# Kernel optimization log

Hardware: AMD Instinct MI355X
Metric: run time of the kernel (lower is better)

Reference implementation:

```python
import jax, jax.numpy as jnp
import numpy as np

F_FRAMES = 128   # number of frames (seq_start_end rows)
P_PEDS = 32      # pedestrians per frame (uniform)
B = F_FRAMES * P_PEDS
E, H, BN, PM, M = 64, 128, 1024, 512, 1024
PRED_LEN = 12


def setup_inputs() -> dict:
    key = jax.random.key(0)
    ks = jax.random.split(key, 20)
    n = lambda k, s, sc=0.05: (jax.random.normal(k, s) * sc).astype(jnp.float32)
    starts = jnp.arange(F_FRAMES, dtype=jnp.int32) * P_PEDS
    seq_start_end = jnp.stack([starts, starts + P_PEDS], axis=1)
    return {
        "h0": n(ks[0], (1, B, H), 1.0),
        "c0": n(ks[1], (1, B, H), 1.0),
        "obs_final_pos": n(ks[2], (B, 2), 1.0),
        "obs_final_pos_rel": n(ks[3], (B, 2), 1.0),
        "W_emb": n(ks[4], (2, E)), "b_emb": jnp.zeros((E,), jnp.float32),
        "W_ih": n(ks[5], (4 * H, E)), "W_hh": n(ks[6], (4 * H, H)),
        "b_ih": jnp.zeros((4 * H,), jnp.float32), "b_hh": jnp.zeros((4 * H,), jnp.float32),
        "W_pos": n(ks[7], (H, 2)), "b_pos": jnp.zeros((2,), jnp.float32),
        "W_pe": n(ks[8], (2, E)), "b_pe": jnp.zeros((E,), jnp.float32),
        "W_p1": n(ks[9], (E + H, PM)), "b_p1": jnp.zeros((PM,), jnp.float32),
        "W_p2": n(ks[10], (PM, BN)), "b_p2": jnp.zeros((BN,), jnp.float32),
        "W_m1": n(ks[11], (H + BN, M)), "b_m1": jnp.zeros((M,), jnp.float32),
        "W_m2": n(ks[12], (M, H)), "b_m2": jnp.zeros((H,), jnp.float32),
        "seq_start_end": seq_start_end,
    }


def reference(h0, c0, obs_final_pos, obs_final_pos_rel,
              W_emb, b_emb, W_ih, W_hh, b_ih, b_hh, W_pos, b_pos,
              W_pe, b_pe, W_p1, b_p1, W_p2, b_p2, W_m1, b_m1, W_m2, b_m2,
              seq_start_end):
    Bn = h0.shape[1]
    F = seq_start_end.shape[0]
    P = Bn // F  # uniform frame size
    h, c = h0[0], c0[0]
    x0 = obs_final_pos_rel @ W_emb + b_emb  # decoder input embedding

    def step(carry, _):
        x, h, c, last_pos = carry
        # LSTM cell (PyTorch gate order i,f,g,o)
        gates = x @ W_ih.T + h @ W_hh.T + b_ih + b_hh  # (B, 4H)
        i, f, g, o = jnp.split(gates, 4, axis=-1)
        i, f, o = jax.nn.sigmoid(i), jax.nn.sigmoid(f), jax.nn.sigmoid(o)
        c_new = f * c + i * jnp.tanh(g)
        h_new = o * jnp.tanh(c_new)
        rel_pos = h_new @ W_pos + b_pos
        curr_pos = rel_pos + last_pos
        # PoolNet: per-frame pairwise rel-pos embed + MLP + max over neighbours j
        pos = curr_pos.reshape(F, P, 2)
        hf = h_new.reshape(F, P, H)
        rel = pos[:, None, :, :] - pos[:, :, None, :]  # rel[f,i,j] = pos_j - pos_i
        e = rel @ W_pe + b_pe  # (F,P,P,E)
        feat = jnp.concatenate(
            [e, jnp.broadcast_to(hf[:, None], (F, P, P, H))], axis=-1)  # h of j
        z = jax.nn.relu(feat @ W_p1 + b_p1)
        z = jax.nn.relu(z @ W_p2 + b_p2)  # (F,P,P,BN)
        pool_h = z.max(axis=2).reshape(Bn, BN)
        # hidden refresh MLP
        mi = jnp.concatenate([h_new, pool_h], axis=-1)
        nh = jax.nn.relu(mi @ W_m1 + b_m1)
        nh = jax.nn.relu(nh @ W_m2 + b_m2)
        x_new = rel_pos @ W_emb + b_emb
        return (x_new, nh, c_new, curr_pos), (curr_pos, rel_pos)

    _, (pred_seq, pred_seq_rel) = jax.lax.scan(
        jax.checkpoint(step), (x0, h, c, obs_final_pos), None, length=PRED_LEN)
    return pred_seq, pred_seq_rel
```

## Files before the change

### kernel.cpp

```cpp
#include <hip/hip_runtime.h>

#define NB 4096
#define HD 128
#define ED 64
#define NF 128
#define NP 32
#define TSTEPS 12

typedef __attribute__((ext_vector_type(8))) short short8;
typedef __attribute__((ext_vector_type(8))) __bf16 bf16x8;
typedef __attribute__((ext_vector_type(8))) _Float16 f16x8;
typedef __attribute__((ext_vector_type(4))) float f32x4;
typedef __attribute__((ext_vector_type(16))) float f32x16;

#define MFMA16(a, b, c)  __builtin_amdgcn_mfma_f32_16x16x32_bf16((a), (b), (c), 0, 0, 0)
#define MFMA32H(a, b, c) __builtin_amdgcn_mfma_f32_32x32x16_f16((a), (b), (c), 0, 0, 0)

__device__ __forceinline__ unsigned short f2bf(float f) {
  unsigned int x = __float_as_uint(f);
  x += 0x7fffu + ((x >> 16) & 1u);
  return (unsigned short)(x >> 16);
}

__device__ __forceinline__ float sigm(float x) { return 1.0f / (1.0f + expf(-x)); }

__device__ __forceinline__ f16x8 relu8(f16x8 x) {
  return __builtin_elementwise_max(x, (f16x8)(_Float16)0);
}


__global__ __launch_bounds__(256) void k_transpose_bf(const float* __restrict__ W,
                                                      unsigned short* __restrict__ Wt,
                                                      int K, int N) {
  __shared__ float t[32][33];
  int nb = blockIdx.x * 32, kb = blockIdx.y * 32;
  int tx = threadIdx.x & 31, ty = threadIdx.x >> 5;
  #pragma unroll
  for (int r = 0; r < 32; r += 8)
    t[ty + r][tx] = W[(size_t)(kb + ty + r) * N + nb + tx];
  __syncthreads();
  #pragma unroll
  for (int r = 0; r < 32; r += 8)
    Wt[(size_t)(nb + ty + r) * K + kb + tx] = f2bf(t[tx][ty + r]);
}

__global__ __launch_bounds__(256) void k_pack_bfrag32(const float* __restrict__ Wp2,
                                                      _Float16* __restrict__ Bf) {
  int U = blockIdx.x * 256 + threadIdx.x;
  int l = U & 63, cb = (U >> 6) & 31, ks = U >> 11;
  int col = cb * 32 + (l & 31);
  int k0 = ks * 16 + (l >> 5) * 8;
  f16x8 r;
  #pragma unroll
  for (int e = 0; e < 8; ++e) r[e] = (_Float16)Wp2[(size_t)(k0 + e) * 1024 + col];
  *(f16x8*)(Bf + (size_t)U * 8) = r;
}

__global__ __launch_bounds__(256) void k_pack_lstm_w(const float* __restrict__ Wih,
                                                     const float* __restrict__ Whh,
                                                     float* __restrict__ WihT,
                                                     float* __restrict__ WhhT) {
  int idx = blockIdx.x * 256 + threadIdx.x;
  if (idx < 64 * 512) { int k = idx >> 9, n = idx & 511; WihT[idx] = Wih[n * 64 + k]; }
  if (idx < 128 * 512) { int k = idx >> 9, n = idx & 511; WhhT[idx] = Whh[n * 128 + k]; }
}

__global__ __launch_bounds__(256) void k_pack_wpp(const float* __restrict__ Wpe,
                                                  const float* __restrict__ bpe,
                                                  const float* __restrict__ Wp1,
                                                  const float* __restrict__ bp1,
                                                  float* __restrict__ Wpp,
                                                  float* __restrict__ cvec) {
  int n = blockIdx.x * 256 + threadIdx.x;
  if (n >= 512) return;
  float s0 = 0.f, s1 = 0.f, sc = 0.f;
  for (int k = 0; k < 64; ++k) {
    float w = Wp1[k * 512 + n];
    s0 += Wpe[k] * w;
    s1 += Wpe[64 + k] * w;
    sc += bpe[k] * w;
  }
  Wpp[n * 2] = s0; Wpp[n * 2 + 1] = s1; cvec[n] = sc + bp1[n];
}

__global__ __launch_bounds__(256) void k_x0(const float* __restrict__ ofr,
                                            const float* __restrict__ Wemb,
                                            const float* __restrict__ bemb,
                                            float* __restrict__ x) {
  int idx = blockIdx.x * 256 + threadIdx.x;
  if (idx >= NB * ED) return;
  int row = idx >> 6, e = idx & 63;
  x[idx] = bemb[e] + ofr[row * 2] * Wemb[e] + ofr[row * 2 + 1] * Wemb[64 + e];
}


__global__ __launch_bounds__(256) void k12_lstm_uv(
    const float* __restrict__ x, const float* __restrict__ hin, const float* __restrict__ cin,
    const float* __restrict__ WihT, const float* __restrict__ WhhT,
    const float* __restrict__ bih, const float* __restrict__ bhh,
    const float* __restrict__ Wpos, const float* __restrict__ bpos,
    const float* __restrict__ Wemb, const float* __restrict__ bemb,
    const float* __restrict__ lastpos,
    const float* __restrict__ Wp1, const float* __restrict__ Wpp,
    const float* __restrict__ cvec,
    float* __restrict__ cout, unsigned short* __restrict__ mi,
    float* __restrict__ posout, float* __restrict__ xout,
    float* __restrict__ outc, float* __restrict__ outr,
    _Float16* __restrict__ u16, _Float16* __restrict__ v16) {
  __shared__ float xh[8][192];
  __shared__ float hnl[8][128];
  __shared__ float rp[8][2];
  __shared__ float cp[8][2];
  int tid = threadIdx.x;
  int r0 = blockIdx.x * 8;
  for (int idx = tid; idx < 8 * 192; idx += 256) {
    int r = idx / 192, k = idx % 192;
    xh[r][k] = (k < 64) ? x[(r0 + r) * 64 + k] : hin[(r0 + r) * 128 + (k - 64)];
  }
  __syncthreads();
  int j = tid & 127, rg = tid >> 7;
  float acc0[4], acc1[4], acc2[4], acc3[4];
  {
    float b0 = bih[j] + bhh[j];
    float b1 = bih[128 + j] + bhh[128 + j];
    float b2 = bih[256 + j] + bhh[256 + j];
    float b3 = bih[384 + j] + bhh[384 + j];
    #pragma unroll
    for (int r = 0; r < 4; ++r) { acc0[r] = b0; acc1[r] = b1; acc2[r] = b2; acc3[r] = b3; }
  }
  for (int k = 0; k < 64; ++k) {
    float w0 = WihT[k * 512 + j], w1 = WihT[k * 512 + 128 + j],
          w2 = WihT[k * 512 + 256 + j], w3 = WihT[k * 512 + 384 + j];
    #pragma unroll
    for (int r = 0; r < 4; ++r) {
      float xv = xh[rg * 4 + r][k];
      acc0[r] += w0 * xv; acc1[r] += w1 * xv; acc2[r] += w2 * xv; acc3[r] += w3 * xv;
    }
  }
  for (int k = 0; k < 128; ++k) {
    float w0 = WhhT[k * 512 + j], w1 = WhhT[k * 512 + 128 + j],
          w2 = WhhT[k * 512 + 256 + j], w3 = WhhT[k * 512 + 384 + j];
    #pragma unroll
    for (int r = 0; r < 4; ++r) {
      float hv = xh[rg * 4 + r][64 + k];
      acc0[r] += w0 * hv; acc1[r] += w1 * hv; acc2[r] += w2 * hv; acc3[r] += w3 * hv;
    }
  }
  #pragma unroll
  for (int r = 0; r < 4; ++r) {
    int row = r0 + rg * 4 + r;
    float ig = sigm(acc0[r]), fg = sigm(acc1[r]), gg = tanhf(acc2[r]), og = sigm(acc3[r]);
    float cn = fg * cin[row * 128 + j] + ig * gg;
    float hv = og * tanhf(cn);
    cout[row * 128 + j] = cn;
    mi[(size_t)row * 1152 + j] = f2bf(hv);
    hnl[rg * 4 + r][j] = hv;
  }
  __syncthreads();
  {
    int r = tid >> 5;
    int d = (tid >> 4) & 1;
    int l = tid & 15;
    float s = 0.f;
    #pragma unroll
    for (int k = l; k < 128; k += 16) s += hnl[r][k] * Wpos[k * 2 + d];
    s += __shfl_xor(s, 1);
    s += __shfl_xor(s, 2);
    s += __shfl_xor(s, 4);
    s += __shfl_xor(s, 8);
    if (l == 0) {
      int row = r0 + r;
      float rel = s + bpos[d];
      float cur = rel + lastpos[row * 2 + d];
      rp[r][d] = rel;
      cp[r][d] = cur;
      posout[row * 2 + d] = cur;
      outc[row * 2 + d] = cur;
      outr[row * 2 + d] = rel;
    }
  }
  __syncthreads();
  for (int idx = tid; idx < 8 * 64; idx += 256) {
    int r = idx >> 6, e = idx & 63;
    xout[(r0 + r) * 64 + e] = bemb[e] + rp[r][0] * Wemb[e] + rp[r][1] * Wemb[64 + e];
  }
  int n = tid, n2 = tid + 256;
  float aA[8], aB[8];
  #pragma unroll
  for (int r = 0; r < 8; ++r) { aA[r] = 0.f; aB[r] = 0.f; }
  for (int k = 0; k < 128; ++k) {
    float wA = Wp1[(64 + k) * 512 + n], wB = Wp1[(64 + k) * 512 + n2];
    #pragma unroll
    for (int r = 0; r < 8; ++r) { aA[r] += wA * hnl[r][k]; aB[r] += wB * hnl[r][k]; }
  }
  float wp0A = Wpp[n * 2], wp1A = Wpp[n * 2 + 1], cA = cvec[n];
  float wp0B = Wpp[n2 * 2], wp1B = Wpp[n2 * 2 + 1], cB = cvec[n2];
  #pragma unroll
  for (int r = 0; r < 8; ++r) {
    int row = r0 + r;
    float t0 = cp[r][0] * wp0A + cp[r][1] * wp1A;
    v16[(size_t)row * 512 + n] = (_Float16)t0;
    u16[(size_t)row * 512 + n] = (_Float16)(t0 + aA[r] + cA);
    float t1 = cp[r][0] * wp0B + cp[r][1] * wp1B;
    v16[(size_t)row * 512 + n2] = (_Float16)t1;
    u16[(size_t)row * 512 + n2] = (_Float16)(t1 + aB[r] + cB);
  }
}

__global__ __launch_bounds__(512, 4) void k3_pool(
    const _Float16* __restrict__ u16, const _Float16* __restrict__ v16,
    const _Float16* __restrict__ Bf, const float* __restrict__ bp2,
    unsigned short* __restrict__ mi) {
  __shared__ _Float16 u_lds[32 * 512];
  __shared__ _Float16 v_lds[8 * 512];
  int f = blockIdx.x, ig = blockIdx.y, ng = blockIdx.z;
  int tid = threadIdx.x, wid = tid >> 6, lane = tid & 63;
  int r32 = lane & 31, hi = lane >> 5;
  int ip = wid >> 1, nh = wid & 1;

  const f16x8* Bfu = (const f16x8*)Bf;
  int cb0 = ng * 4 + nh * 2;

  f16x8 Bb[4][2];
  #pragma unroll
  for (int s = 0; s < 3; ++s) {
    Bb[s][0] = Bfu[(size_t)((s * 32 + cb0 + 0) * 64 + lane)];
    Bb[s][1] = Bfu[(size_t)((s * 32 + cb0 + 1) * 64 + lane)];
  }

  #pragma unroll
  for (int t = 0; t < 4; ++t) {
    int unit = tid + t * 512;
    int row = unit >> 6, seg = unit & 63;
    f16x8 val = *(const f16x8*)(u16 + (size_t)(f * 32 + row) * 512 + seg * 8);
    int byte = (row << 10) + (seg << 4);
    byte ^= (row & 7) << 4;
    *(f16x8*)((char*)u_lds + byte) = val;
  }
  {
    int row = tid >> 6, seg = tid & 63;
    *(f16x8*)(v_lds + (row << 9) + seg * 8) =
        *(const f16x8*)(v16 + (size_t)(f * 32 + ig * 8 + row) * 512 + seg * 8);
  }
  __syncthreads();

  f32x16 acc[2][2];
  #pragma unroll
  for (int a = 0; a < 2; ++a)
    #pragma unroll
    for (int n = 0; n < 2; ++n)
      #pragma unroll
      for (int r = 0; r < 16; ++r) acc[a][n][r] = 0.f;

  int ubase = (r32 << 10) + (hi << 4);
  int usw = (r32 & 7) << 4;
  const _Float16* vp = v_lds + ((ip * 2) << 9) + hi * 8;

  #pragma unroll
  for (int ks = 0; ks < 32; ++ks) {
    if (ks + 3 < 32) {
      Bb[(ks + 3) & 3][0] = Bfu[(size_t)(((ks + 3) * 32 + cb0 + 0) * 64 + lane)];
      Bb[(ks + 3) & 3][1] = Bfu[(size_t)(((ks + 3) * 32 + cb0 + 1) * 64 + lane)];
    }
    f16x8 uf = *(const f16x8*)((const char*)u_lds + ((ubase + ks * 32) ^ usw));
    f16x8 a0 = relu8(uf - *(const f16x8*)(vp + ks * 16));
    f16x8 a1 = relu8(uf - *(const f16x8*)(vp + 512 + ks * 16));
    __builtin_amdgcn_s_setprio(1);
    acc[0][0] = MFMA32H(a0, Bb[ks & 3][0], acc[0][0]);
    acc[1][0] = MFMA32H(a1, Bb[ks & 3][0], acc[1][0]);
    acc[0][1] = MFMA32H(a0, Bb[ks & 3][1], acc[0][1]);
    acc[1][1] = MFMA32H(a1, Bb[ks & 3][1], acc[1][1]);
    __builtin_amdgcn_s_setprio(0);
  }

  #pragma unroll
  for (int ii = 0; ii < 2; ++ii) {
    int rowg = f * 32 + ig * 8 + ip * 2 + ii;
    #pragma unroll
    for (int nt = 0; nt < 2; ++nt) {
      float m = acc[ii][nt][0];
      #pragma unroll
      for (int r = 1; r < 16; ++r) m = fmaxf(m, acc[ii][nt][r]);
      m = fmaxf(m, __shfl_xor(m, 32));
      if (hi == 0) {
        int col = (cb0 + nt) * 32 + r32;
        float val = fmaxf(m + bp2[col], 0.f);
        mi[(size_t)rowg * 1152 + 128 + col] = f2bf(val);
      }
    }
  }
}

__global__ __launch_bounds__(512) void k4_mlp1(
    const unsigned short* __restrict__ mi, const unsigned short* __restrict__ Wt,
    const float* __restrict__ bm1, unsigned short* __restrict__ nh1) {
  int bid = blockIdx.x;
  int mb = bid & 63, nb = bid >> 6;
  int tid = threadIdx.x, wid = tid >> 6, lane = tid & 63;
  int row0 = mb * 64 + (wid >> 2) * 32;
  int nc0 = nb * 256 + (wid & 3) * 64;
  int c = lane & 15, q = lane >> 4;
  const unsigned short* a0p = mi + (size_t)(row0 + c) * 1152;
  const unsigned short* a1p = a0p + 16 * 1152;
  const unsigned short* bb = Wt + (size_t)(nc0 + c) * 1152;
  f32x4 acc[2][4];
  #pragma unroll
  for (int a = 0; a < 2; ++a)
    #pragma unroll
    for (int b = 0; b < 4; ++b) acc[a][b] = (f32x4){0.f, 0.f, 0.f, 0.f};
  for (int ks = 0; ks < 36; ++ks) {
    int k0 = ks * 32 + q * 8;
    bf16x8 a0 = *(const bf16x8*)(a0p + k0);
    bf16x8 a1 = *(const bf16x8*)(a1p + k0);
    #pragma unroll
    for (int nt = 0; nt < 4; ++nt) {
      bf16x8 bf = *(const bf16x8*)(bb + (size_t)nt * 16 * 1152 + k0);
      acc[0][nt] = MFMA16(a0, bf, acc[0][nt]);
      acc[1][nt] = MFMA16(a1, bf, acc[1][nt]);
    }
  }
  #pragma unroll
  for (int mt = 0; mt < 2; ++mt)
    #pragma unroll
    for (int nt = 0; nt < 4; ++nt)
      #pragma unroll
      for (int r = 0; r < 4; ++r) {
        int row = row0 + mt * 16 + q * 4 + r;
        int col = nc0 + nt * 16 + c;
        float val = fmaxf(acc[mt][nt][r] + bm1[col], 0.f);
        nh1[(size_t)row * 1024 + col] = f2bf(val);
      }
}

__global__ __launch_bounds__(128) void k5_mlp2(
    const unsigned short* __restrict__ nh1, const unsigned short* __restrict__ Wt,
    const float* __restrict__ bm2, float* __restrict__ hout) {
  int bid = blockIdx.x;
  int tid = threadIdx.x, wid = tid >> 6, lane = tid & 63;
  int row0 = bid * 16;
  int nc0 = wid * 64;
  int c = lane & 15, q = lane >> 4;
  const unsigned short* ap = nh1 + (size_t)(row0 + c) * 1024;
  const unsigned short* bb = Wt + (size_t)(nc0 + c) * 1024;
  f32x4 acc[4];
  #pragma unroll
  for (int b = 0; b < 4; ++b) acc[b] = (f32x4){0.f, 0.f, 0.f, 0.f};
  for (int ks = 0; ks < 32; ++ks) {
    int k0 = ks * 32 + q * 8;
    bf16x8 a = *(const bf16x8*)(ap + k0);
    #pragma unroll
    for (int nt = 0; nt < 4; ++nt) {
      bf16x8 bf = *(const bf16x8*)(bb + (size_t)nt * 16 * 1024 + k0);
      acc[nt] = MFMA16(a, bf, acc[nt]);
    }
  }
  #pragma unroll
  for (int nt = 0; nt < 4; ++nt)
    #pragma unroll
    for (int r = 0; r < 4; ++r) {
      int row = row0 + q * 4 + r;
      int col = nc0 + nt * 16 + c;
      hout[(size_t)row * 128 + col] = fmaxf(acc[nt][r] + bm2[col], 0.f);
    }
}


extern "C" void kernel_launch(void* const* d_in, const int* in_sizes, int n_in,
                              void* d_out, int out_size, void* d_ws, size_t ws_size,
                              hipStream_t stream) {
  const float* h0   = (const float*)d_in[0];
  const float* c0   = (const float*)d_in[1];
  const float* ofp  = (const float*)d_in[2];
  const float* ofr  = (const float*)d_in[3];
  const float* Wemb = (const float*)d_in[4];
  const float* bemb = (const float*)d_in[5];
  const float* Wih  = (const float*)d_in[6];
  const float* Whh  = (const float*)d_in[7];
  const float* bih  = (const float*)d_in[8];
  const float* bhh  = (const float*)d_in[9];
  const float* Wpos = (const float*)d_in[10];
  const float* bpos = (const float*)d_in[11];
  const float* Wpe  = (const float*)d_in[12];
  const float* bpe  = (const float*)d_in[13];
  const float* Wp1  = (const float*)d_in[14];
  const float* bp1  = (const float*)d_in[15];
  const float* Wp2  = (const float*)d_in[16];
  const float* bp2  = (const float*)d_in[17];
  const float* Wm1  = (const float*)d_in[18];
  const float* bm1  = (const float*)d_in[19];
  const float* Wm2  = (const float*)d_in[20];
  const float* bm2  = (const float*)d_in[21];

  char* ws = (char*)d_ws;
  size_t off = 0;
  auto alloc = [&](size_t bytes) {
    char* p = ws + off;
    off += (bytes + 255) & ~(size_t)255;
    return p;
  };
  float* h    = (float*)alloc((size_t)NB * HD * 4);
  float* cst  = (float*)alloc((size_t)NB * HD * 4);
  float* xbuf = (float*)alloc((size_t)NB * ED * 4);
  float* pos  = (float*)alloc((size_t)NB * 2 * 4);
  _Float16* u16 = (_Float16*)alloc((size_t)NB * 512 * 2);
  _Float16* v16 = (_Float16*)alloc((size_t)NB * 512 * 2);
  unsigned short* mi   = (unsigned short*)alloc((size_t)NB * 1152 * 2);
  unsigned short* nh1  = (unsigned short*)alloc((size_t)NB * 1024 * 2);
  float* WihT = (float*)alloc(64 * 512 * 4);
  float* WhhT = (float*)alloc(128 * 512 * 4);
  float* Wpp  = (float*)alloc(512 * 2 * 4);
  float* cvec = (float*)alloc(512 * 4);
  _Float16* Bf  = (_Float16*)alloc((size_t)1024 * 512 * 2);
  unsigned short* Wm1t = (unsigned short*)alloc((size_t)1024 * 1152 * 2);
  unsigned short* Wm2t = (unsigned short*)alloc((size_t)128 * 1024 * 2);

  float* outc = (float*)d_out;
  float* outr = outc + (size_t)TSTEPS * NB * 2;

  k_pack_lstm_w<<<256, 256, 0, stream>>>(Wih, Whh, WihT, WhhT);
  k_pack_wpp<<<2, 256, 0, stream>>>(Wpe, bpe, Wp1, bp1, Wpp, cvec);
  k_pack_bfrag32<<<256, 256, 0, stream>>>(Wp2, Bf);
  k_transpose_bf<<<dim3(1024 / 32, 1152 / 32), 256, 0, stream>>>(Wm1, Wm1t, 1152, 1024);
  k_transpose_bf<<<dim3(128 / 32, 1024 / 32), 256, 0, stream>>>(Wm2, Wm2t, 1024, 128);
  k_x0<<<NB * ED / 256, 256, 0, stream>>>(ofr, Wemb, bemb, xbuf);

  for (int t = 0; t < TSTEPS; ++t) {
    const float* hin = (t == 0) ? h0 : h;
    const float* cin = (t == 0) ? c0 : cst;
    const float* lp  = (t == 0) ? ofp : pos;
    k12_lstm_uv<<<NB / 8, 256, 0, stream>>>(xbuf, hin, cin, WihT, WhhT, bih, bhh,
                                            Wpos, bpos, Wemb, bemb, lp, Wp1, Wpp, cvec,
                                            cst, mi, pos, xbuf,
                                            outc + (size_t)t * NB * 2,
                                            outr + (size_t)t * NB * 2, u16, v16);
    k3_pool<<<dim3(128, 4, 8), 512, 0, stream>>>(u16, v16, Bf, bp2, mi);
    k4_mlp1<<<256, 512, 0, stream>>>(mi, Wm1t, bm1, nh1);
    k5_mlp2<<<256, 128, 0, stream>>>(nh1, Wm2t, bm2, h);
  }
}
```

Before: 2.990 ms.

## Fuse hidden-refresh MLP layers into one kernel and prefetch pool LDS operands

Merges the two hidden-refresh GEMM kernels into a single kernel per 16-row block. The 1024-wide intermediate stays in shared memory instead of being written to and reread from global memory, which also removes one launch per step. Each block now computes all 1024 first-layer columns for 16 rows, so the block count drops and every block streams the full Wm1 matrix, which may hurt weight reuse and parallelism. Separately, the pool kernel's inner loop now loads the next iteration's u/v LDS fragments one step ahead to hide LDS latency.

```diff
diff --git a/kernel.cpp b/kernel.cpp
--- a/kernel.cpp
+++ b/kernel.cpp
@@ -256,21 +256,31 @@
   int usw = (r32 & 7) << 4;
   const _Float16* vp = v_lds + ((ip * 2) << 9) + hi * 8;
 
+  f16x8 ufc = *(const f16x8*)((const char*)u_lds + (ubase ^ usw));
+  f16x8 v0c = *(const f16x8*)(vp);
+  f16x8 v1c = *(const f16x8*)(vp + 512);
+
   #pragma unroll
   for (int ks = 0; ks < 32; ++ks) {
+    f16x8 ufn, v0n, v1n;
+    if (ks + 1 < 32) {
+      ufn = *(const f16x8*)((const char*)u_lds + ((ubase + (ks + 1) * 32) ^ usw));
+      v0n = *(const f16x8*)(vp + (ks + 1) * 16);
+      v1n = *(const f16x8*)(vp + 512 + (ks + 1) * 16);
+    }
     if (ks + 3 < 32) {
       Bb[(ks + 3) & 3][0] = Bfu[(size_t)(((ks + 3) * 32 + cb0 + 0) * 64 + lane)];
       Bb[(ks + 3) & 3][1] = Bfu[(size_t)(((ks + 3) * 32 + cb0 + 1) * 64 + lane)];
     }
-    f16x8 uf = *(const f16x8*)((const char*)u_lds + ((ubase + ks * 32) ^ usw));
-    f16x8 a0 = relu8(uf - *(const f16x8*)(vp + ks * 16));
-    f16x8 a1 = relu8(uf - *(const f16x8*)(vp + 512 + ks * 16));
+    f16x8 a0 = relu8(ufc - v0c);
+    f16x8 a1 = relu8(ufc - v1c);
     __builtin_amdgcn_s_setprio(1);
     acc[0][0] = MFMA32H(a0, Bb[ks & 3][0], acc[0][0]);
     acc[1][0] = MFMA32H(a1, Bb[ks & 3][0], acc[1][0]);
     acc[0][1] = MFMA32H(a0, Bb[ks & 3][1], acc[0][1]);
     acc[1][1] = MFMA32H(a1, Bb[ks & 3][1], acc[1][1]);
     __builtin_amdgcn_s_setprio(0);
+    if (ks + 1 < 32) { ufc = ufn; v0c = v0n; v1c = v1n; }
   }
 
   #pragma unroll
@@ -291,77 +301,62 @@
   }
 }
 
-__global__ __launch_bounds__(512) void k4_mlp1(
-    const unsigned short* __restrict__ mi, const unsigned short* __restrict__ Wt,
-    const float* __restrict__ bm1, unsigned short* __restrict__ nh1) {
+__global__ __launch_bounds__(512) void k45_mlp(
+    const unsigned short* __restrict__ mi, const unsigned short* __restrict__ Wm1t,
+    const float* __restrict__ bm1, const unsigned short* __restrict__ Wm2t,
+    const float* __restrict__ bm2, float* __restrict__ hout) {
+  __shared__ unsigned short nh1_lds[16 * 1032];
   int bid = blockIdx.x;
-  int mb = bid & 63, nb = bid >> 6;
   int tid = threadIdx.x, wid = tid >> 6, lane = tid & 63;
-  int row0 = mb * 64 + (wid >> 2) * 32;
-  int nc0 = nb * 256 + (wid & 3) * 64;
   int c = lane & 15, q = lane >> 4;
-  const unsigned short* a0p = mi + (size_t)(row0 + c) * 1152;
-  const unsigned short* a1p = a0p + 16 * 1152;
-  const unsigned short* bb = Wt + (size_t)(nc0 + c) * 1152;
-  f32x4 acc[2][4];
-  #pragma unroll
-  for (int a = 0; a < 2; ++a)
-    #pragma unroll
-    for (int b = 0; b < 4; ++b) acc[a][b] = (f32x4){0.f, 0.f, 0.f, 0.f};
-  for (int ks = 0; ks < 36; ++ks) {
-    int k0 = ks * 32 + q * 8;
-    bf16x8 a0 = *(const bf16x8*)(a0p + k0);
-    bf16x8 a1 = *(const bf16x8*)(a1p + k0);
-    #pragma unroll
-    for (int nt = 0; nt < 4; ++nt) {
-      bf16x8 bf = *(const bf16x8*)(bb + (size_t)nt * 16 * 1152 + k0);
-      acc[0][nt] = MFMA16(a0, bf, acc[0][nt]);
-      acc[1][nt] = MFMA16(a1, bf, acc[1][nt]);
-    }
-  }
-  #pragma unroll
-  for (int mt = 0; mt < 2; ++mt)
-    #pragma unroll
-    for (int nt = 0; nt < 4; ++nt)
+  int row0 = bid * 16;
+
+  {
+    int nc0 = wid * 128;
+    const unsigned short* a0p = mi + (size_t)(row0 + c) * 1152;
+    const unsigned short* bb = Wm1t + (size_t)(nc0 + c) * 1152;
+    f32x4 acc[8];
+    #pragma unroll
+    for (int b = 0; b < 8; ++b) acc[b] = (f32x4){0.f, 0.f, 0.f, 0.f};
+    for (int ks = 0; ks < 36; ++ks) {
+      int k0 = ks * 32 + q * 8;
+      bf16x8 a0 = *(const bf16x8*)(a0p + k0);
+      #pragma unroll
+      for (int nt = 0; nt < 8; ++nt) {
+        bf16x8 bf = *(const bf16x8*)(bb + (size_t)nt * 16 * 1152 + k0);
+        acc[nt] = MFMA16(a0, bf, acc[nt]);
+      }
+    }
+    #pragma unroll
+    for (int nt = 0; nt < 8; ++nt)
       #pragma unroll
       for (int r = 0; r < 4; ++r) {
-        int row = row0 + mt * 16 + q * 4 + r;
+        int row = q * 4 + r;
         int col = nc0 + nt * 16 + c;
-        float val = fmaxf(acc[mt][nt][r] + bm1[col], 0.f);
-        nh1[(size_t)row * 1024 + col] = f2bf(val);
+        float val = fmaxf(acc[nt][r] + bm1[col], 0.f);
+        nh1_lds[row * 1032 + col] = f2bf(val);
       }
-}
-
-__global__ __launch_bounds__(128) void k5_mlp2(
-    const unsigned short* __restrict__ nh1, const unsigned short* __restrict__ Wt,
-    const float* __restrict__ bm2, float* __restrict__ hout) {
-  int bid = blockIdx.x;
-  int tid = threadIdx.x, wid = tid >> 6, lane = tid & 63;
-  int row0 = bid * 16;
-  int nc0 = wid * 64;
-  int c = lane & 15, q = lane >> 4;
-  const unsigned short* ap = nh1 + (size_t)(row0 + c) * 1024;
-  const unsigned short* bb = Wt + (size_t)(nc0 + c) * 1024;
-  f32x4 acc[4];
-  #pragma unroll
-  for (int b = 0; b < 4; ++b) acc[b] = (f32x4){0.f, 0.f, 0.f, 0.f};
-  for (int ks = 0; ks < 32; ++ks) {
-    int k0 = ks * 32 + q * 8;
-    bf16x8 a = *(const bf16x8*)(ap + k0);
-    #pragma unroll
-    for (int nt = 0; nt < 4; ++nt) {
-      bf16x8 bf = *(const bf16x8*)(bb + (size_t)nt * 16 * 1024 + k0);
-      acc[nt] = MFMA16(a, bf, acc[nt]);
-    }
-  }
-  #pragma unroll
-  for (int nt = 0; nt < 4; ++nt)
+  }
+  __syncthreads();
+
+  {
+    int nc0 = wid * 16;
+    const unsigned short* ap = nh1_lds + c * 1032;
+    const unsigned short* bb = Wm2t + (size_t)(nc0 + c) * 1024;
+    f32x4 acc = (f32x4){0.f, 0.f, 0.f, 0.f};
+    for (int ks = 0; ks < 32; ++ks) {
+      int k0 = ks * 32 + q * 8;
+      bf16x8 a = *(const bf16x8*)(ap + k0);
+      bf16x8 bf = *(const bf16x8*)(bb + k0);
+      acc = MFMA16(a, bf, acc);
+    }
     #pragma unroll
     for (int r = 0; r < 4; ++r) {
       int row = row0 + q * 4 + r;
-      int col = nc0 + nt * 16 + c;
-      hout[(size_t)row * 128 + col] = fmaxf(acc[nt][r] + bm2[col], 0.f);
-    }
+      int col = nc0 + c;
+      hout[(size_t)row * 128 + col] = fmaxf(acc[r] + bm2[col], 0.f);
+    }
+  }
 }
 
 
@@ -405,7 +400,6 @@
   _Float16* u16 = (_Float16*)alloc((size_t)NB * 512 * 2);
   _Float16* v16 = (_Float16*)alloc((size_t)NB * 512 * 2);
   unsigned short* mi   = (unsigned short*)alloc((size_t)NB * 1152 * 2);
-  unsigned short* nh1  = (unsigned short*)alloc((size_t)NB * 1024 * 2);
   float* WihT = (float*)alloc(64 * 512 * 4);
   float* WhhT = (float*)alloc(128 * 512 * 4);
   float* Wpp  = (float*)alloc(512 * 2 * 4);
@@ -434,7 +428,6 @@
                                             outc + (size_t)t * NB * 2,
                                             outr + (size_t)t * NB * 2, u16, v16);
     k3_pool<<<dim3(128, 4, 8), 512, 0, stream>>>(u16, v16, Bf, bp2, mi);
-    k4_mlp1<<<256, 512, 0, stream>>>(mi, Wm1t, bm1, nh1);
-    k5_mlp2<<<256, 128, 0, stream>>>(nh1, Wm2t, bm2, h);
-  }
-}
+    k45_mlp<<<256, 512, 0, stream>>>(mi, Wm1t, bm1, Wm2t, bm2, h);
+  }
+}
```

Result: slower. 3.545 ms (+18.6%).
